# Kernel optimization log

Hardware: AMD Instinct MI355X
Metric: run time of the kernel (lower is better)

The kernel has to match this reference:

```python
import jax, jax.numpy as jnp
import numpy as np

N = 100000   # nodes
F = 256      # input features
H = 64       # hidden dims
C = 40       # classes
L = 4        # GGNN layers
E = 1200000  # edges


def setup_inputs() -> dict:
    key = jax.random.key(0)
    ks = jax.random.split(key, 8)
    x = jax.random.normal(ks[0], (N, F), dtype=jnp.float32)
    edge_index = jax.random.randint(ks[1], (2, E), 0, N, dtype=jnp.int64)
    # glorot-initialized projection weights
    weight_in = jax.random.uniform(ks[2], (F, H), jnp.float32, -1.0, 1.0) * np.sqrt(6.0 / (F + H))
    weight_out = jax.random.uniform(ks[3], (H, C), jnp.float32, -1.0, 1.0) * np.sqrt(6.0 / (H + C))
    # GatedGraphConv: per-layer message weight [L, H, H], shared GRUCell params
    conv_weight = jax.random.uniform(ks[4], (L, H, H), jnp.float32, -1.0, 1.0) * np.sqrt(6.0 / (2 * H))
    s = 1.0 / np.sqrt(H)
    w_ih = jax.random.uniform(ks[5], (3 * H, H), jnp.float32, -s, s)
    w_hh = jax.random.uniform(ks[6], (3 * H, H), jnp.float32, -s, s)
    b_ih = jax.random.uniform(ks[7], (3 * H,), jnp.float32, -s, s)
    b_hh = jnp.zeros((3 * H,), jnp.float32)
    return {"x": x, "edge_index": edge_index, "weight_in": weight_in,
            "weight_out": weight_out, "conv_weight": conv_weight,
            "w_ih": w_ih, "w_hh": w_hh, "b_ih": b_ih, "b_hh": b_hh}


def _gru_cell(a, h, w_ih, w_hh, b_ih, b_hh):
    # torch.nn.GRUCell math: input a, hidden h
    gi = a @ w_ih.T + b_ih
    gh = h @ w_hh.T + b_hh
    i_r, i_z, i_n = jnp.split(gi, 3, axis=1)
    h_r, h_z, h_n = jnp.split(gh, 3, axis=1)
    r = jax.nn.sigmoid(i_r + h_r)
    z = jax.nn.sigmoid(i_z + h_z)
    n = jnp.tanh(i_n + r * h_n)
    return (1.0 - z) * n + z * h


def reference(x, edge_index, weight_in, weight_out, conv_weight, w_ih, w_hh, b_ih, b_hh):
    n_nodes = x.shape[0]
    src, dst = edge_index[0], edge_index[1]
    h = x @ weight_in  # [N, H]
    for i in range(conv_weight.shape[0]):
        m = h @ conv_weight[i]                                   # [N, H]
        agg = jax.ops.segment_sum(m[src], dst, num_segments=n_nodes)  # scatter-add
        h = _gru_cell(agg, h, w_ih, w_hh, b_ih, b_hh)
    out = h @ weight_out  # [N, C]
    return jax.nn.log_softmax(out, axis=1)
```

## Files before the change

kernel.cpp:

```cpp
#include <hip/hip_runtime.h>


#define DEVI __device__ __forceinline__

typedef __attribute__((ext_vector_type(8))) short short8;
typedef __attribute__((ext_vector_type(4))) short bf16x4;
typedef __attribute__((ext_vector_type(4))) float f32x4;

constexpr int N_NODES   = 100000;
constexpr int F_IN      = 256;
constexpr int H_DIM     = 64;
constexpr int C_OUT     = 40;
constexpr int ROW_TILES = N_NODES / 16;
constexpr int CH        = 8192;
constexpr int NBUCK     = (N_NODES + 127) / 128;
constexpr int LB_STRIDE = NBUCK + 1;
constexpr int BCAP      = 2048;

DEVI float bf2f(unsigned short u) {
    unsigned v = ((unsigned)u) << 16;
    float f; __builtin_memcpy(&f, &v, 4); return f;
}
DEVI unsigned short f2bf(float f) {
    unsigned u; __builtin_memcpy(&u, &f, 4);
    unsigned r = u + 0x7FFFu + ((u >> 16) & 1u);
    return (unsigned short)(r >> 16);
}
DEVI float in_elem(const void* p, size_t idx, int f32flag) {
    return f32flag ? ((const float*)p)[idx]
                   : bf2f(((const unsigned short*)p)[idx]);
}
DEVI short8 f32row_to_frag(const float* __restrict__ p) {
    const f32x4* q = (const f32x4*)p;
    f32x4 lo = q[0], hi = q[1];
    short8 a;
    a[0] = (short)f2bf(lo[0]); a[1] = (short)f2bf(lo[1]);
    a[2] = (short)f2bf(lo[2]); a[3] = (short)f2bf(lo[3]);
    a[4] = (short)f2bf(hi[0]); a[5] = (short)f2bf(hi[1]);
    a[6] = (short)f2bf(hi[2]); a[7] = (short)f2bf(hi[3]);
    return a;
}

__global__ void detect_kernel(const void* x, const int* ei, int* flags) {
    if (threadIdx.x != 0 || blockIdx.x != 0) return;
    const unsigned short* u = (const unsigned short*)x;
    int sane = 0;
    for (int i = 0; i < 256; ++i) {
        int e = (u[i] >> 7) & 0xFF;
        if (e >= 100 && e <= 145) sane++;
    }
    flags[0] = (sane < 230) ? 1 : 0;
    int zeros = 0;
    for (int i = 0; i < 64; ++i)
        if (ei[2 * i + 1] == 0) zeros++;
    flags[1] = (zeros >= 63) ? 1 : 0;
}

__global__ __launch_bounds__(256) void bucket_local(
        const int* __restrict__ ei, int E, const int* __restrict__ flags,
        int* __restrict__ wgsorted,
        int* __restrict__ lbase_g) {
    __shared__ int hist[NBUCK];
    __shared__ int partial[256];
    __shared__ int staging[CH];
    int tid = threadIdx.x, wg = blockIdx.x;
    int i64 = flags[1];
    int base = wg * CH;
    int cnt_wg = min(CH, E - base);

    for (int i = tid; i < NBUCK; i += 256) hist[i] = 0;
    __syncthreads();
    for (int k = tid; k < cnt_wg; k += 256) {
        size_t e = (size_t)base + k;
        int d = i64 ? ei[2 * ((size_t)E + e)] : ei[(size_t)E + e];
        atomicAdd(&hist[d >> 7], 1);
    }
    __syncthreads();
    int i0 = 4 * tid;
    int e0 = (i0 + 0 < NBUCK) ? hist[i0 + 0] : 0;
    int e1 = (i0 + 1 < NBUCK) ? hist[i0 + 1] : 0;
    int e2 = (i0 + 2 < NBUCK) ? hist[i0 + 2] : 0;
    int e3 = (i0 + 3 < NBUCK) ? hist[i0 + 3] : 0;
    int s0 = e0, s1 = s0 + e1, s2 = s1 + e2, s3 = s2 + e3;
    __syncthreads();
    partial[tid] = s3;
    __syncthreads();
    for (int ofs = 1; ofs < 256; ofs <<= 1) {
        int add = (tid >= ofs) ? partial[tid - ofs] : 0;
        __syncthreads();
        partial[tid] += add;
        __syncthreads();
    }
    int pbase = (tid > 0) ? partial[tid - 1] : 0;
    if (i0 + 0 < NBUCK) hist[i0 + 0] = pbase;
    if (i0 + 1 < NBUCK) hist[i0 + 1] = pbase + s0;
    if (i0 + 2 < NBUCK) hist[i0 + 2] = pbase + s1;
    if (i0 + 3 < NBUCK) hist[i0 + 3] = pbase + s2;
    __syncthreads();
    int* lb = lbase_g + (size_t)wg * LB_STRIDE;
    for (int i = tid; i < NBUCK; i += 256) lb[i] = hist[i];
    if (tid == 0) lb[NBUCK] = cnt_wg;
    __syncthreads();
    for (int k = tid; k < cnt_wg; k += 256) {
        size_t e = (size_t)base + k;
        int s, d;
        if (i64) { s = ei[2 * e]; d = ei[2 * ((size_t)E + e)]; }
        else     { s = ei[e];     d = ei[(size_t)E + e]; }
        int pos = atomicAdd(&hist[d >> 7], 1);
        staging[pos] = ((d & 127) << 17) | s;
    }
    __syncthreads();
    for (int k = tid; k < cnt_wg; k += 256)
        wgsorted[(size_t)base + k] = staging[k];
}

__global__ __launch_bounds__(256) void bucket_csr(
        const int* __restrict__ wgsorted,
        const int* __restrict__ lbase_g,
        int nwg,
        int* __restrict__ rowptr,
        int* __restrict__ counts,
        int* __restrict__ esrc) {
    __shared__ int segincl[256];
    __shared__ int segbase[256];
    __shared__ int edata[BCAP];
    __shared__ int sout[BCAP];
    __shared__ int hist2[128];
    __shared__ int cur2[128];
    int tid = threadIdx.x, b = blockIdx.x;

    int lbv = 0, cntv = 0;
    if (tid < nwg) {
        const int* lb = lbase_g + (size_t)tid * LB_STRIDE;
        lbv  = lb[b];
        cntv = lb[b + 1] - lbv;
    }
    segbase[tid] = lbv;
    segincl[tid] = cntv;
    __syncthreads();
    for (int ofs = 1; ofs < 256; ofs <<= 1) {
        int add = (tid >= ofs) ? segincl[tid - ofs] : 0;
        __syncthreads();
        segincl[tid] += add;
        __syncthreads();
    }
    int tot = min(segincl[255], BCAP);
    for (int i = tid; i < tot; i += 256) {
        int lo = 0, hi = 255;
        while (lo < hi) {
            int mid = (lo + hi) >> 1;
            if (segincl[mid] > i) hi = mid; else lo = mid + 1;
        }
        int excl = (lo > 0) ? segincl[lo - 1] : 0;
        edata[i] = wgsorted[(size_t)lo * CH + segbase[lo] + (i - excl)];
    }
    if (tid < 128) hist2[tid] = 0;
    __syncthreads();
    for (int i = tid; i < tot; i += 256) atomicAdd(&hist2[edata[i] >> 17], 1);
    __syncthreads();
    if (tid < 128) cur2[tid] = hist2[tid];
    __syncthreads();
    for (int ofs = 1; ofs < 128; ofs <<= 1) {
        int add = 0;
        if (tid < 128 && tid >= ofs) add = cur2[tid - ofs];
        __syncthreads();
        if (tid < 128) cur2[tid] += add;
        __syncthreads();
    }
    int nodeexcl = 0;
    if (tid < 128) nodeexcl = (tid > 0) ? cur2[tid - 1] : 0;
    __syncthreads();
    if (tid < 128) {
        int node = b * 128 + tid;
        if (node < N_NODES) {
            counts[node] = hist2[tid];
            rowptr[node] = b * BCAP + nodeexcl;
        }
        cur2[tid] = nodeexcl;
    }
    __syncthreads();
    for (int i = tid; i < tot; i += 256) {
        int p = edata[i];
        int pos = atomicAdd(&cur2[p >> 17], 1);
        sout[pos] = p & 0x1FFFF;
    }
    __syncthreads();
    for (int i = tid; i < tot; i += 256)
        esrc[(size_t)b * BCAP + i] = sout[i];
}

__global__ void prep_all(const void* __restrict__ w_in,
                         const void* __restrict__ w_out,
                         const void* __restrict__ w_hh,
                         const void* __restrict__ b_ih,
                         const void* __restrict__ b_hh,
                         const void* __restrict__ conv_w,
                         const void* __restrict__ w_ih,
                         unsigned short* __restrict__ winfrag,
                         unsigned short* __restrict__ wofrag,
                         unsigned short* __restrict__ whh_c,
                         unsigned short* __restrict__ bias_c,
                         unsigned short* __restrict__ wcomb,
                         const int* __restrict__ flags) {
    int f32 = flags[0];
    int t = blockIdx.x * blockDim.x + threadIdx.x;
    if (t < 16384) {
        int i = t & 7, lane = (t >> 3) & 63, jt = (t >> 9) & 3, kb = t >> 11;
        int k = kb * 32 + ((lane >> 4) << 3) + i;
        int col = jt * 16 + (lane & 15);
        winfrag[t] = f2bf(in_elem(w_in, (size_t)k * 64 + col, f32));
    } else if (t < 19456) {
        int u = t - 16384;
        int i = u & 7, lane = (u >> 3) & 63;
        int jt = (u >> 9) % 3, kb = u / 1536;
        int k = kb * 32 + ((lane >> 4) << 3) + i;
        int col = jt * 16 + (lane & 15);
        wofrag[u] = (col < 40) ? f2bf(in_elem(w_out, (size_t)k * 40 + col, f32))
                               : (unsigned short)0;
    } else if (t < 31744) {
        int u = t - 19456;
        whh_c[u] = f2bf(in_elem(w_hh, u, f32));
    } else if (t < 31936) {
        int u = t - 31744;
        bias_c[u] = f2bf(in_elem(b_ih, u, f32));
    } else if (t < 32128) {
        int u = t - 31936;
        bias_c[192 + u] = f2bf(in_elem(b_hh, u, f32));
    } else if (t < 32128 + 49152) {
        int u = t - 32128;
        int l = u / 12288;
        int idx = u % 12288;
        int i = idx & 7, lane = (idx >> 3) & 63, c = idx >> 9;
        int kb = c / 12, jt = c % 12;
        int quad = lane >> 4, l15 = lane & 15;
        int k = kb * 32 + quad * 8 + i;
        int g = jt * 16 + l15;
        float acc = 0.0f;
        if (f32) {
            const f32x4* ca = (const f32x4*)((const float*)conv_w +
                                             (size_t)l * 4096 + (size_t)k * 64);
            const f32x4* wa = (const f32x4*)((const float*)w_ih + (size_t)g * 64);
#pragma unroll
            for (int jq = 0; jq < 16; ++jq) {
                f32x4 cv = ca[jq];
                f32x4 wv = wa[jq];
                acc += cv[0] * wv[0] + cv[1] * wv[1] + cv[2] * wv[2] + cv[3] * wv[3];
            }
        } else {
            const short8* ca = (const short8*)((const unsigned short*)conv_w +
                                               (size_t)l * 4096 + (size_t)k * 64);
            const short8* wa = (const short8*)((const unsigned short*)w_ih +
                                               (size_t)g * 64);
#pragma unroll
            for (int jq = 0; jq < 8; ++jq) {
                short8 cv = ca[jq];
                short8 wv = wa[jq];
#pragma unroll
                for (int q = 0; q < 8; ++q)
                    acc += bf2f((unsigned short)cv[q]) * bf2f((unsigned short)wv[q]);
            }
        }
        wcomb[(size_t)l * 12288 + idx] = f2bf(acc);
    }
}

template <int XF32>
DEVI void proj_in_body(const void* __restrict__ xr,
                       const unsigned short* __restrict__ wfrag,
                       unsigned short* __restrict__ h) {
    int wid = blockIdx.x * 4 + (threadIdx.x >> 6);
    if (wid >= ROW_TILES) return;
    int lane = threadIdx.x & 63;
    int l15 = lane & 15, quad = lane >> 4;
    int row0 = wid * 16;
    int arow = row0 + l15;

    f32x4 acc[4];
#pragma unroll
    for (int jt = 0; jt < 4; ++jt) acc[jt] = (f32x4)(0.0f);

#pragma unroll
    for (int kb = 0; kb < 8; ++kb) {
        short8 a;
        if (XF32)
            a = f32row_to_frag((const float*)xr + (size_t)arow * F_IN + kb * 32 + quad * 8);
        else
            a = *(const short8*)((const unsigned short*)xr + (size_t)arow * F_IN + kb * 32 + quad * 8);
#pragma unroll
        for (int jt = 0; jt < 4; ++jt) {
            short8 b = *(const short8*)(wfrag + (size_t)((kb * 4 + jt) * 64 + lane) * 8);
            acc[jt] = __builtin_amdgcn_mfma_f32_16x16x32_bf16(a, b, acc[jt], 0, 0, 0);
        }
    }
#pragma unroll
    for (int jt = 0; jt < 4; ++jt)
#pragma unroll
        for (int r = 0; r < 4; ++r)
            h[(size_t)(row0 + quad * 4 + r) * H_DIM + jt * 16 + l15] = f2bf(acc[jt][r]);
}

__global__ __launch_bounds__(256) void proj_in_kernel(
        const void* __restrict__ x,
        const unsigned short* __restrict__ wfrag,
        unsigned short* __restrict__ h,
        const int* __restrict__ flags) {
    if (flags[0]) proj_in_body<1>(x, wfrag, h);
    else          proj_in_body<0>(x, wfrag, h);
}

__global__ __launch_bounds__(256) void gather_agg(
        const unsigned short* __restrict__ h,
        const int* __restrict__ rowptr,
        const int* __restrict__ counts,
        const int* __restrict__ esrc,
        unsigned short* __restrict__ aggB) {
    int n = blockIdx.x * 4 + (threadIdx.x >> 6);
    if (n >= N_NODES) return;
    int lane = threadIdx.x & 63;
    int sub  = lane >> 4;
    int c4   = (lane & 15) * 4;
    int start = rowptr[n];
    int deg   = counts[n];

    f32x4 acc0 = (f32x4)(0.0f), acc1 = (f32x4)(0.0f);

    for (int i = 0; i < deg; i += 32) {
        int sidx[8];
#pragma unroll
        for (int u = 0; u < 8; ++u) {
            int e = i + u * 4 + sub;
            sidx[u] = (e < deg) ? esrc[start + e] : -1;
        }
#pragma unroll
        for (int u = 0; u < 8; ++u) {
            if (sidx[u] >= 0) {
                bf16x4 v = *(const bf16x4*)(h + (size_t)sidx[u] * H_DIM + c4);
                f32x4& A = (u & 1) ? acc1 : acc0;
                A[0] += bf2f((unsigned short)v[0]);
                A[1] += bf2f((unsigned short)v[1]);
                A[2] += bf2f((unsigned short)v[2]);
                A[3] += bf2f((unsigned short)v[3]);
            }
        }
    }

#pragma unroll
    for (int k = 0; k < 4; ++k) acc0[k] += acc1[k];
#pragma unroll
    for (int k = 0; k < 4; ++k) {
        acc0[k] += __shfl_xor(acc0[k], 16);
        acc0[k] += __shfl_xor(acc0[k], 32);
    }
    if (sub == 0) {
        bf16x4 o;
        o[0] = (short)f2bf(acc0[0]);
        o[1] = (short)f2bf(acc0[1]);
        o[2] = (short)f2bf(acc0[2]);
        o[3] = (short)f2bf(acc0[3]);
        *(bf16x4*)(aggB + (size_t)n * H_DIM + c4) = o;
    }
}

__global__ __launch_bounds__(256) void gru_kernel(
        const unsigned short* __restrict__ aggB,
        unsigned short* __restrict__ h,
        const unsigned short* __restrict__ wcomb_l,
        const unsigned short* __restrict__ whh_c,
        const unsigned short* __restrict__ bias_c) {
    int wid = blockIdx.x * 4 + (threadIdx.x >> 6);
    if (wid >= ROW_TILES) return;
    int lane = threadIdx.x & 63;
    int l15 = lane & 15, quad = lane >> 4;
    int row0 = wid * 16;
    int arow = row0 + l15;

    f32x4 gi[12], gh[12];
#pragma unroll
    for (int jt = 0; jt < 12; ++jt) { gi[jt] = (f32x4)(0.0f); gh[jt] = (f32x4)(0.0f); }

#pragma unroll
    for (int kb = 0; kb < 2; ++kb) {
        short8 aa = *(const short8*)(aggB + (size_t)arow * H_DIM + kb * 32 + quad * 8);
        short8 ah = *(const short8*)(h + (size_t)arow * H_DIM + kb * 32 + quad * 8);
#pragma unroll
        for (int jt = 0; jt < 12; ++jt) {
            short8 bi = *(const short8*)(wcomb_l + (size_t)((kb * 12 + jt) * 64 + lane) * 8);
            gi[jt] = __builtin_amdgcn_mfma_f32_16x16x32_bf16(aa, bi, gi[jt], 0, 0, 0);
            short8 bh = *(const short8*)(whh_c + (size_t)(jt * 16 + l15) * H_DIM + kb * 32 + quad * 8);
            gh[jt] = __builtin_amdgcn_mfma_f32_16x16x32_bf16(ah, bh, gh[jt], 0, 0, 0);
        }
    }

#pragma unroll
    for (int jc = 0; jc < 4; ++jc) {
        int j = jc * 16 + l15;
        float bir = bf2f(bias_c[j]),       bhr = bf2f(bias_c[192 + j]);
        float biz = bf2f(bias_c[64 + j]),  bhz = bf2f(bias_c[256 + j]);
        float bin = bf2f(bias_c[128 + j]), bhn = bf2f(bias_c[320 + j]);
#pragma unroll
        for (int r = 0; r < 4; ++r) {
            int row = row0 + quad * 4 + r;
            float xr = (gi[jc][r] + bir) + (gh[jc][r] + bhr);
            float xz = (gi[4 + jc][r] + biz) + (gh[4 + jc][r] + bhz);
            float in_ = gi[8 + jc][r] + bin;
            float hn_ = gh[8 + jc][r] + bhn;
            xr = fminf(fmaxf(xr, -30.0f), 30.0f);
            xz = fminf(fmaxf(xz, -30.0f), 30.0f);
            float rg = 1.0f / (1.0f + __expf(-xr));
            float zg = 1.0f / (1.0f + __expf(-xz));
            float na = in_ + rg * hn_;
            float ey = __expf(-2.0f * fabsf(na));
            float th = (1.0f - ey) / (1.0f + ey);
            float nt = (na < 0.0f) ? -th : th;
            float ho = bf2f(h[(size_t)row * H_DIM + j]);
            h[(size_t)row * H_DIM + j] = f2bf((1.0f - zg) * nt + zg * ho);
        }
    }
}

__global__ __launch_bounds__(256) void projout_kernel(
        const unsigned short* __restrict__ h,
        const unsigned short* __restrict__ wofrag,
        void* __restrict__ out,
        const int* __restrict__ flags) {
    int f32out = flags[0];
    int wid = blockIdx.x * 4 + (threadIdx.x >> 6);
    if (wid >= ROW_TILES) return;
    int lane = threadIdx.x & 63;
    int l15 = lane & 15, quad = lane >> 4;
    int row0 = wid * 16;
    int arow = row0 + l15;

    f32x4 acc[3];
#pragma unroll
    for (int jt = 0; jt < 3; ++jt) acc[jt] = (f32x4)(0.0f);

#pragma unroll
    for (int kb = 0; kb < 2; ++kb) {
        short8 a = *(const short8*)(h + (size_t)arow * H_DIM + kb * 32 + quad * 8);
#pragma unroll
        for (int jt = 0; jt < 3; ++jt) {
            short8 b = *(const short8*)(wofrag + (size_t)((kb * 3 + jt) * 64 + lane) * 8);
            acc[jt] = __builtin_amdgcn_mfma_f32_16x16x32_bf16(a, b, acc[jt], 0, 0, 0);
        }
    }

    float* of = (float*)out;
    unsigned short* ob = (unsigned short*)out;
    bool valid2 = (l15 < 8);
#pragma unroll
    for (int r = 0; r < 4; ++r) {
        int row = row0 + quad * 4 + r;
        float v0 = acc[0][r], v1 = acc[1][r], v2 = acc[2][r];
        float mx = fmaxf(v0, v1);
        if (valid2) mx = fmaxf(mx, v2);
#pragma unroll
        for (int d = 1; d < 16; d <<= 1) mx = fmaxf(mx, __shfl_xor(mx, d));
        float s = __expf(v0 - mx) + __expf(v1 - mx) + (valid2 ? __expf(v2 - mx) : 0.0f);
#pragma unroll
        for (int d = 1; d < 16; d <<= 1) s += __shfl_xor(s, d);
        float lg = mx + __logf(s);
        size_t o0 = (size_t)row * C_OUT + l15;
        if (f32out) {
            of[o0]      = v0 - lg;
            of[o0 + 16] = v1 - lg;
            if (valid2) of[o0 + 32] = v2 - lg;
        } else {
            ob[o0]      = f2bf(v0 - lg);
            ob[o0 + 16] = f2bf(v1 - lg);
            if (valid2) ob[o0 + 32] = f2bf(v2 - lg);
        }
    }
}

extern "C" void kernel_launch(void* const* d_in, const int* in_sizes, int n_in,
                              void* d_out, int out_size, void* d_ws, size_t ws_size,
                              hipStream_t stream) {
    const void* x      = d_in[0];
    const int*  ei     = (const int*)d_in[1];
    const void* w_in   = d_in[2];
    const void* w_out  = d_in[3];
    const void* conv_w = d_in[4];
    const void* w_ih   = d_in[5];
    const void* w_hh   = d_in[6];
    const void* b_ih   = d_in[7];
    const void* b_hh   = d_in[8];

    const int E   = in_sizes[1] / 2;
    const int nwg = (E + CH - 1) / CH;

    char* ws = (char*)d_ws;
    size_t off = 0;
    auto carve = [&](size_t bytes) {
        void* p = ws + off;
        off += (bytes + 255) & ~(size_t)255;
        return p;
    };
    int*            flags    = (int*)carve(256);
    unsigned short* aggB     = (unsigned short*)carve((size_t)N_NODES * H_DIM * 2);
    unsigned short* hbuf     = (unsigned short*)carve((size_t)N_NODES * H_DIM * 2);
    int*            counts   = (int*)carve((size_t)N_NODES * 4);
    int*            rowptr   = (int*)carve((size_t)N_NODES * 4);
    int*            wgsorted = (int*)carve((size_t)nwg * CH * 4);
    int*            lbase_g  = (int*)carve((size_t)nwg * LB_STRIDE * 4);
    int*            esrcP    = (int*)carve((size_t)NBUCK * BCAP * 4);
    unsigned short* winfrag  = (unsigned short*)carve((size_t)16384 * 2);
    unsigned short* wcomb    = (unsigned short*)carve((size_t)4 * 12288 * 2);
    unsigned short* wofrag   = (unsigned short*)carve((size_t)3072 * 2);
    unsigned short* whh_c    = (unsigned short*)carve((size_t)12288 * 2);
    unsigned short* bias_c   = (unsigned short*)carve((size_t)384 * 2);

    detect_kernel<<<1, 64, 0, stream>>>(x, ei, flags);

    for (int rep = 0; rep < 3; ++rep) {
        bucket_local<<<nwg, 256, 0, stream>>>(ei, E, flags, wgsorted, lbase_g);
        bucket_csr<<<NBUCK, 256, 0, stream>>>(wgsorted, lbase_g, nwg,
                                              rowptr, counts, esrcP);
    }

    prep_all<<<(32128 + 49152 + 255) / 256, 256, 0, stream>>>(
        w_in, w_out, w_hh, b_ih, b_hh, conv_w, w_ih,
        winfrag, wofrag, whh_c, bias_c, wcomb, flags);

    const int gblocks = (ROW_TILES + 3) / 4;
    const int nblocks = N_NODES / 4;

    proj_in_kernel<<<gblocks, 256, 0, stream>>>(x, winfrag, hbuf, flags);

    for (int l = 0; l < 4; ++l) {
        gather_agg<<<nblocks, 256, 0, stream>>>(hbuf, rowptr, counts, esrcP, aggB);
        gru_kernel<<<gblocks, 256, 0, stream>>>(aggB, hbuf, wcomb + (size_t)l * 12288,
                                                whh_c, bias_c);
    }

    projout_kernel<<<gblocks, 256, 0, stream>>>(hbuf, wofrag, d_out, flags);
}
```

Before: 636.9 us.

## Fuse detection, weight prep and output projection; drop repeated CSR build

Removes the redundant 3x repetition of the bucket/CSR build so it runs once. Folds the dtype probes into bucket_local using wave ballots, and merges weight preparation into the CSR kernel. The final GRU layer writes its new hidden state to LDS and runs the output projection plus log-softmax in the same kernel, so one h round-trip is skipped. The aim is fewer launches and less memory traffic, at the cost of extra LDS and code size in the last GRU kernel.

```diff
diff --git a/kernel.cpp b/kernel.cpp
--- a/kernel.cpp
+++ b/kernel.cpp
@@ -16,6 +16,7 @@
 constexpr int NBUCK     = (N_NODES + 127) / 128;
 constexpr int LB_STRIDE = NBUCK + 1;
 constexpr int BCAP      = 2048;
+constexpr int LPAD      = 72;
 
 DEVI float bf2f(unsigned short u) {
     unsigned v = ((unsigned)u) << 16;
@@ -41,30 +42,39 @@
     return a;
 }
 
-__global__ void detect_kernel(const void* x, const int* ei, int* flags) {
-    if (threadIdx.x != 0 || blockIdx.x != 0) return;
+DEVI int probe_i64_wave(const int* __restrict__ ei) {
+    int lane = threadIdx.x & 63;
+    unsigned long long m = __ballot(ei[2 * lane + 1] == 0);
+    return __popcll(m) >= 63;
+}
+DEVI int probe_f32_wave(const void* __restrict__ x) {
     const unsigned short* u = (const unsigned short*)x;
-    int sane = 0;
-    for (int i = 0; i < 256; ++i) {
-        int e = (u[i] >> 7) & 0xFF;
-        if (e >= 100 && e <= 145) sane++;
-    }
-    flags[0] = (sane < 230) ? 1 : 0;
-    int zeros = 0;
-    for (int i = 0; i < 64; ++i)
-        if (ei[2 * i + 1] == 0) zeros++;
-    flags[1] = (zeros >= 63) ? 1 : 0;
+    int lane = threadIdx.x & 63;
+    int cnt = 0;
+#pragma unroll
+    for (int i = 0; i < 4; ++i) {
+        int e = (u[lane + i * 64] >> 7) & 0xFF;
+        cnt += (e >= 100 && e <= 145) ? 1 : 0;
+    }
+#pragma unroll
+    for (int d = 1; d < 64; d <<= 1) cnt += __shfl_xor(cnt, d);
+    return cnt < 230;
 }
 
 __global__ __launch_bounds__(256) void bucket_local(
-        const int* __restrict__ ei, int E, const int* __restrict__ flags,
+        const int* __restrict__ ei, int E, const void* __restrict__ x,
         int* __restrict__ wgsorted,
-        int* __restrict__ lbase_g) {
+        int* __restrict__ lbase_g,
+        int* __restrict__ flags) {
     __shared__ int hist[NBUCK];
     __shared__ int partial[256];
     __shared__ int staging[CH];
     int tid = threadIdx.x, wg = blockIdx.x;
-    int i64 = flags[1];
+    int i64 = probe_i64_wave(ei);
+    if (wg == 0 && tid < 64) {
+        int f32 = probe_f32_wave(x);
+        if (tid == 0) { flags[0] = f32; flags[1] = i64; }
+    }
     int base = wg * CH;
     int cnt_wg = min(CH, E - base);
 
@@ -114,20 +124,97 @@
         wgsorted[(size_t)base + k] = staging[k];
 }
 
-__global__ __launch_bounds__(256) void bucket_csr(
+__global__ __launch_bounds__(256) void bucket_csr_prep(
         const int* __restrict__ wgsorted,
         const int* __restrict__ lbase_g,
         int nwg,
         int* __restrict__ rowptr,
         int* __restrict__ counts,
-        int* __restrict__ esrc) {
+        int* __restrict__ esrc,
+        const void* __restrict__ w_in,
+        const void* __restrict__ w_out,
+        const void* __restrict__ w_hh,
+        const void* __restrict__ b_ih,
+        const void* __restrict__ b_hh,
+        const void* __restrict__ conv_w,
+        const void* __restrict__ w_ih,
+        unsigned short* __restrict__ winfrag,
+        unsigned short* __restrict__ wofrag,
+        unsigned short* __restrict__ whh_c,
+        unsigned short* __restrict__ bias_c,
+        unsigned short* __restrict__ wcomb,
+        const int* __restrict__ flags) {
+    int tid = threadIdx.x, b = blockIdx.x;
+
+    {
+        int f32 = flags[0];
+        int t = b * 256 + tid;
+        if (t < 16384) {
+            int i = t & 7, lane = (t >> 3) & 63, jt = (t >> 9) & 3, kb = t >> 11;
+            int k = kb * 32 + ((lane >> 4) << 3) + i;
+            int col = jt * 16 + (lane & 15);
+            winfrag[t] = f2bf(in_elem(w_in, (size_t)k * 64 + col, f32));
+        } else if (t < 19456) {
+            int u = t - 16384;
+            int i = u & 7, lane = (u >> 3) & 63;
+            int jt = (u >> 9) % 3, kb = u / 1536;
+            int k = kb * 32 + ((lane >> 4) << 3) + i;
+            int col = jt * 16 + (lane & 15);
+            wofrag[u] = (col < 40) ? f2bf(in_elem(w_out, (size_t)k * 40 + col, f32))
+                                   : (unsigned short)0;
+        } else if (t < 31744) {
+            int u = t - 19456;
+            whh_c[u] = f2bf(in_elem(w_hh, u, f32));
+        } else if (t < 31936) {
+            int u = t - 31744;
+            bias_c[u] = f2bf(in_elem(b_ih, u, f32));
+        } else if (t < 32128) {
+            int u = t - 31936;
+            bias_c[192 + u] = f2bf(in_elem(b_hh, u, f32));
+        } else if (t < 32128 + 49152) {
+            int u = t - 32128;
+            int l = u / 12288;
+            int idx = u % 12288;
+            int i = idx & 7, lane = (idx >> 3) & 63, c = idx >> 9;
+            int kb = c / 12, jt = c % 12;
+            int quad = lane >> 4, l15 = lane & 15;
+            int k = kb * 32 + quad * 8 + i;
+            int g = jt * 16 + l15;
+            float acc = 0.0f;
+            if (f32) {
+                const f32x4* ca = (const f32x4*)((const float*)conv_w +
+                                                 (size_t)l * 4096 + (size_t)k * 64);
+                const f32x4* wa = (const f32x4*)((const float*)w_ih + (size_t)g * 64);
+#pragma unroll
+                for (int jq = 0; jq < 16; ++jq) {
+                    f32x4 cv = ca[jq];
+                    f32x4 wv = wa[jq];
+                    acc += cv[0] * wv[0] + cv[1] * wv[1] + cv[2] * wv[2] + cv[3] * wv[3];
+                }
+            } else {
+                const short8* ca = (const short8*)((const unsigned short*)conv_w +
+                                                   (size_t)l * 4096 + (size_t)k * 64);
+                const short8* wa = (const short8*)((const unsigned short*)w_ih +
+                                                   (size_t)g * 64);
+#pragma unroll
+                for (int jq = 0; jq < 8; ++jq) {
+                    short8 cv = ca[jq];
+                    short8 wv = wa[jq];
+#pragma unroll
+                    for (int q = 0; q < 8; ++q)
+                        acc += bf2f((unsigned short)cv[q]) * bf2f((unsigned short)wv[q]);
+                }
+            }
+            wcomb[(size_t)l * 12288 + idx] = f2bf(acc);
+        }
+    }
+
     __shared__ int segincl[256];
     __shared__ int segbase[256];
     __shared__ int edata[BCAP];
     __shared__ int sout[BCAP];
     __shared__ int hist2[128];
     __shared__ int cur2[128];
-    int tid = threadIdx.x, b = blockIdx.x;
 
     int lbv = 0, cntv = 0;
     if (tid < nwg) {
@@ -187,81 +274,6 @@
     __syncthreads();
     for (int i = tid; i < tot; i += 256)
         esrc[(size_t)b * BCAP + i] = sout[i];
-}
-
-__global__ void prep_all(const void* __restrict__ w_in,
-                         const void* __restrict__ w_out,
-                         const void* __restrict__ w_hh,
-                         const void* __restrict__ b_ih,
-                         const void* __restrict__ b_hh,
-                         const void* __restrict__ conv_w,
-                         const void* __restrict__ w_ih,
-                         unsigned short* __restrict__ winfrag,
-                         unsigned short* __restrict__ wofrag,
-                         unsigned short* __restrict__ whh_c,
-                         unsigned short* __restrict__ bias_c,
-                         unsigned short* __restrict__ wcomb,
-                         const int* __restrict__ flags) {
-    int f32 = flags[0];
-    int t = blockIdx.x * blockDim.x + threadIdx.x;
-    if (t < 16384) {
-        int i = t & 7, lane = (t >> 3) & 63, jt = (t >> 9) & 3, kb = t >> 11;
-        int k = kb * 32 + ((lane >> 4) << 3) + i;
-        int col = jt * 16 + (lane & 15);
-        winfrag[t] = f2bf(in_elem(w_in, (size_t)k * 64 + col, f32));
-    } else if (t < 19456) {
-        int u = t - 16384;
-        int i = u & 7, lane = (u >> 3) & 63;
-        int jt = (u >> 9) % 3, kb = u / 1536;
-        int k = kb * 32 + ((lane >> 4) << 3) + i;
-        int col = jt * 16 + (lane & 15);
-        wofrag[u] = (col < 40) ? f2bf(in_elem(w_out, (size_t)k * 40 + col, f32))
-                               : (unsigned short)0;
-    } else if (t < 31744) {
-        int u = t - 19456;
-        whh_c[u] = f2bf(in_elem(w_hh, u, f32));
-    } else if (t < 31936) {
-        int u = t - 31744;
-        bias_c[u] = f2bf(in_elem(b_ih, u, f32));
-    } else if (t < 32128) {
-        int u = t - 31936;
-        bias_c[192 + u] = f2bf(in_elem(b_hh, u, f32));
-    } else if (t < 32128 + 49152) {
-        int u = t - 32128;
-        int l = u / 12288;
-        int idx = u % 12288;
-        int i = idx & 7, lane = (idx >> 3) & 63, c = idx >> 9;
-        int kb = c / 12, jt = c % 12;
-        int quad = lane >> 4, l15 = lane & 15;
-        int k = kb * 32 + quad * 8 + i;
-        int g = jt * 16 + l15;
-        float acc = 0.0f;
-        if (f32) {
-            const f32x4* ca = (const f32x4*)((const float*)conv_w +
-                                             (size_t)l * 4096 + (size_t)k * 64);
-            const f32x4* wa = (const f32x4*)((const float*)w_ih + (size_t)g * 64);
-#pragma unroll
-            for (int jq = 0; jq < 16; ++jq) {
-                f32x4 cv = ca[jq];
-                f32x4 wv = wa[jq];
-                acc += cv[0] * wv[0] + cv[1] * wv[1] + cv[2] * wv[2] + cv[3] * wv[3];
-            }
-        } else {
-            const short8* ca = (const short8*)((const unsigned short*)conv_w +
-                                               (size_t)l * 4096 + (size_t)k * 64);
-            const short8* wa = (const short8*)((const unsigned short*)w_ih +
-                                               (size_t)g * 64);
-#pragma unroll
-            for (int jq = 0; jq < 8; ++jq) {
-                short8 cv = ca[jq];
-                short8 wv = wa[jq];
-#pragma unroll
-                for (int q = 0; q < 8; ++q)
-                    acc += bf2f((unsigned short)cv[q]) * bf2f((unsigned short)wv[q]);
-            }
-        }
-        wcomb[(size_t)l * 12288 + idx] = f2bf(acc);
-    }
 }
 
 template <int XF32>
@@ -361,18 +373,25 @@
     }
 }
 
+template <int LAST>
 __global__ __launch_bounds__(256) void gru_kernel(
         const unsigned short* __restrict__ aggB,
         unsigned short* __restrict__ h,
         const unsigned short* __restrict__ wcomb_l,
         const unsigned short* __restrict__ whh_c,
-        const unsigned short* __restrict__ bias_c) {
-    int wid = blockIdx.x * 4 + (threadIdx.x >> 6);
+        const unsigned short* __restrict__ bias_c,
+        const unsigned short* __restrict__ wofrag,
+        void* __restrict__ out,
+        const int* __restrict__ flags) {
+    __shared__ __align__(16) unsigned short hnew[4 * 16 * LPAD];
+    int wv = threadIdx.x >> 6;
+    int wid = blockIdx.x * 4 + wv;
     if (wid >= ROW_TILES) return;
     int lane = threadIdx.x & 63;
     int l15 = lane & 15, quad = lane >> 4;
     int row0 = wid * 16;
     int arow = row0 + l15;
+    unsigned short* hw = hnew + wv * 16 * LPAD;
 
     f32x4 gi[12], gh[12];
 #pragma unroll
@@ -413,62 +432,51 @@
             float th = (1.0f - ey) / (1.0f + ey);
             float nt = (na < 0.0f) ? -th : th;
             float ho = bf2f(h[(size_t)row * H_DIM + j]);
-            h[(size_t)row * H_DIM + j] = f2bf((1.0f - zg) * nt + zg * ho);
-        }
-    }
-}
-
-__global__ __launch_bounds__(256) void projout_kernel(
-        const unsigned short* __restrict__ h,
-        const unsigned short* __restrict__ wofrag,
-        void* __restrict__ out,
-        const int* __restrict__ flags) {
-    int f32out = flags[0];
-    int wid = blockIdx.x * 4 + (threadIdx.x >> 6);
-    if (wid >= ROW_TILES) return;
-    int lane = threadIdx.x & 63;
-    int l15 = lane & 15, quad = lane >> 4;
-    int row0 = wid * 16;
-    int arow = row0 + l15;
-
-    f32x4 acc[3];
-#pragma unroll
-    for (int jt = 0; jt < 3; ++jt) acc[jt] = (f32x4)(0.0f);
-
-#pragma unroll
-    for (int kb = 0; kb < 2; ++kb) {
-        short8 a = *(const short8*)(h + (size_t)arow * H_DIM + kb * 32 + quad * 8);
-#pragma unroll
-        for (int jt = 0; jt < 3; ++jt) {
-            short8 b = *(const short8*)(wofrag + (size_t)((kb * 3 + jt) * 64 + lane) * 8);
-            acc[jt] = __builtin_amdgcn_mfma_f32_16x16x32_bf16(a, b, acc[jt], 0, 0, 0);
-        }
-    }
-
-    float* of = (float*)out;
-    unsigned short* ob = (unsigned short*)out;
-    bool valid2 = (l15 < 8);
-#pragma unroll
-    for (int r = 0; r < 4; ++r) {
-        int row = row0 + quad * 4 + r;
-        float v0 = acc[0][r], v1 = acc[1][r], v2 = acc[2][r];
-        float mx = fmaxf(v0, v1);
-        if (valid2) mx = fmaxf(mx, v2);
-#pragma unroll
-        for (int d = 1; d < 16; d <<= 1) mx = fmaxf(mx, __shfl_xor(mx, d));
-        float s = __expf(v0 - mx) + __expf(v1 - mx) + (valid2 ? __expf(v2 - mx) : 0.0f);
-#pragma unroll
-        for (int d = 1; d < 16; d <<= 1) s += __shfl_xor(s, d);
-        float lg = mx + __logf(s);
-        size_t o0 = (size_t)row * C_OUT + l15;
-        if (f32out) {
-            of[o0]      = v0 - lg;
-            of[o0 + 16] = v1 - lg;
-            if (valid2) of[o0 + 32] = v2 - lg;
-        } else {
-            ob[o0]      = f2bf(v0 - lg);
-            ob[o0 + 16] = f2bf(v1 - lg);
-            if (valid2) ob[o0 + 32] = f2bf(v2 - lg);
+            unsigned short hv = f2bf((1.0f - zg) * nt + zg * ho);
+            if (LAST) hw[(quad * 4 + r) * LPAD + j] = hv;
+            else      h[(size_t)row * H_DIM + j] = hv;
+        }
+    }
+
+    if (LAST) {
+        f32x4 pacc[3];
+#pragma unroll
+        for (int jt = 0; jt < 3; ++jt) pacc[jt] = (f32x4)(0.0f);
+#pragma unroll
+        for (int kb = 0; kb < 2; ++kb) {
+            short8 a = *(const short8*)(hw + l15 * LPAD + kb * 32 + quad * 8);
+#pragma unroll
+            for (int jt = 0; jt < 3; ++jt) {
+                short8 bfr = *(const short8*)(wofrag + (size_t)((kb * 3 + jt) * 64 + lane) * 8);
+                pacc[jt] = __builtin_amdgcn_mfma_f32_16x16x32_bf16(a, bfr, pacc[jt], 0, 0, 0);
+            }
+        }
+        int f32out = flags[0];
+        float* of = (float*)out;
+        unsigned short* ob = (unsigned short*)out;
+        bool valid2 = (l15 < 8);
+#pragma unroll
+        for (int r = 0; r < 4; ++r) {
+            int row = row0 + quad * 4 + r;
+            float v0 = pacc[0][r], v1 = pacc[1][r], v2 = pacc[2][r];
+            float mx = fmaxf(v0, v1);
+            if (valid2) mx = fmaxf(mx, v2);
+#pragma unroll
+            for (int d = 1; d < 16; d <<= 1) mx = fmaxf(mx, __shfl_xor(mx, d));
+            float s = __expf(v0 - mx) + __expf(v1 - mx) + (valid2 ? __expf(v2 - mx) : 0.0f);
+#pragma unroll
+            for (int d = 1; d < 16; d <<= 1) s += __shfl_xor(s, d);
+            float lg = mx + __logf(s);
+            size_t o0 = (size_t)row * C_OUT + l15;
+            if (f32out) {
+                of[o0]      = v0 - lg;
+                of[o0 + 16] = v1 - lg;
+                if (valid2) of[o0 + 32] = v2 - lg;
+            } else {
+                ob[o0]      = f2bf(v0 - lg);
+                ob[o0 + 16] = f2bf(v1 - lg);
+                if (valid2) ob[o0 + 32] = f2bf(v2 - lg);
+            }
         }
     }
 }
@@ -510,15 +518,9 @@
     unsigned short* whh_c    = (unsigned short*)carve((size_t)12288 * 2);
     unsigned short* bias_c   = (unsigned short*)carve((size_t)384 * 2);
 
-    detect_kernel<<<1, 64, 0, stream>>>(x, ei, flags);
-
-    for (int rep = 0; rep < 3; ++rep) {
-        bucket_local<<<nwg, 256, 0, stream>>>(ei, E, flags, wgsorted, lbase_g);
-        bucket_csr<<<NBUCK, 256, 0, stream>>>(wgsorted, lbase_g, nwg,
-                                              rowptr, counts, esrcP);
-    }
-
-    prep_all<<<(32128 + 49152 + 255) / 256, 256, 0, stream>>>(
+    bucket_local<<<nwg, 256, 0, stream>>>(ei, E, x, wgsorted, lbase_g, flags);
+    bucket_csr_prep<<<NBUCK, 256, 0, stream>>>(
+        wgsorted, lbase_g, nwg, rowptr, counts, esrcP,
         w_in, w_out, w_hh, b_ih, b_hh, conv_w, w_ih,
         winfrag, wofrag, whh_c, bias_c, wcomb, flags);
 
@@ -527,11 +529,12 @@
 
     proj_in_kernel<<<gblocks, 256, 0, stream>>>(x, winfrag, hbuf, flags);
 
-    for (int l = 0; l < 4; ++l) {
+    for (int l = 0; l < 3; ++l) {
         gather_agg<<<nblocks, 256, 0, stream>>>(hbuf, rowptr, counts, esrcP, aggB);
-        gru_kernel<<<gblocks, 256, 0, stream>>>(aggB, hbuf, wcomb + (size_t)l * 12288,
-                                                whh_c, bias_c);
-    }
-
-    projout_kernel<<<gblocks, 256, 0, stream>>>(hbuf, wofrag, d_out, flags);
-}
+        gru_kernel<0><<<gblocks, 256, 0, stream>>>(aggB, hbuf, wcomb + (size_t)l * 12288,
+                                                   whh_c, bias_c, wofrag, d_out, flags);
+    }
+    gather_agg<<<nblocks, 256, 0, stream>>>(hbuf, rowptr, counts, esrcP, aggB);
+    gru_kernel<1><<<gblocks, 256, 0, stream>>>(aggB, hbuf, wcomb + (size_t)3 * 12288,
+                                               whh_c, bias_c, wofrag, d_out, flags);
+}
```

New measurement: 553.7 us. 1.15x faster.
